# Kernel tuning notes

Measured on AMD Instinct MI355X. Metric: run time of the kernel, lower is better.

Reference implementation:

```python
import jax, jax.numpy as jnp
from jax import lax
import numpy as np

# Module hyperparameters (match init_kwargs)
N = 4            # number of multiplex cells per feature map
NUM_FM = 64      # feature maps in the input
NF = N * NUM_FM  # lateral channel count = 256
H = W = 32       # feature map height/width
D = 2            # lateral neighborhood radius
PRD = 2          # padding repair distance (must equal D for symmetric pad)
KS = 2 * D + 1   # lateral kernel size = 5
IOTA = 0.1       # blend of activation vs lateral support for winner selection
B = 16           # batch size


def minmax_fm(x):
    """Min-max normalize each feature map (over the last two dims) to [0,1].
    Degenerate (constant) maps map to 0."""
    mn = jnp.min(x, axis=(-2, -1), keepdims=True)
    mx = jnp.max(x, axis=(-2, -1), keepdims=True)
    denom = mx - mn
    safe = jnp.where(denom > 0, denom, 1.0)
    return jnp.where(denom > 0, (x - mn) / safe, 0.0)


def _pad(A):
    # pad_activations: zeros of shape (.., PRD+D+H, PRD+D+W), A at [PRD:-PRD]
    # with PRD == D this is symmetric (PRD, D) padding.
    return jnp.pad(A, ((0, 0), (0, 0), (PRD, D), (PRD, D)))


def _conv(x, w):
    # x: (B, Cin, H', W'), w: (Cout, Cin, KS, KS) -> VALID conv (padding=0)
    return lax.conv_general_dilated(x, w, (1, 1), 'VALID',
                                    dimension_numbers=('NCHW', 'OIHW', 'NCHW'))


def setup_inputs() -> dict:
    key = jax.random.key(0)
    k1, k2 = jax.random.split(key)
    A = jax.random.uniform(k1, (B, NUM_FM, H, W), dtype=jnp.float32)
    K = jax.random.normal(k2, (NF, NF, KS, KS), dtype=jnp.float32)  # trained lateral kernel
    S = jnp.ones((NF,), dtype=jnp.float32)                          # scaling param
    return {"A": A, "K": K, "S": S}


def reference(A, K, S):
    batch = A.shape[0]
    # A.repeat(1, n, 1, 1): tile input n times along channels -> (B, NF, H, W)
    A_rep = jnp.tile(A, (1, N, 1, 1))

    # First lateral pass: conv with minmax-normalized K^T, scaled by S, minmaxed.
    L1 = _conv(_pad(A_rep), minmax_fm(jnp.swapaxes(K, 0, 1))) / NUM_FM
    L1 = L1 * S[None, :, None, None]
    L1 = minmax_fm(L1)

    # Winner-take-all multiplex selection (deterministic branch):
    s = jnp.sum((1.0 - IOTA) * A_rep + IOTA * L1, axis=(-2, -1))  # (B, NF)
    s = jnp.swapaxes(s.reshape(batch, N, NUM_FM), 1, 2)            # (B, NUM_FM, N)
    A_max = jnp.argmax(s, axis=-1)                                  # (B, NUM_FM)
    fm_idx = NUM_FM * A_max + jnp.arange(NUM_FM)                    # (B, NUM_FM) channel ids

    # Active-channel mask (complement = inactive_multiplex_idx in the original)
    active = jnp.zeros((batch, NF), dtype=bool)
    active = active.at[jnp.arange(batch)[:, None], fm_idx].set(True)

    # Zero inactive channels of A (tmp_A) and diagonal K[i,i] for inactive i
    # (large_K[b, idx, idx] = 0 is pairwise/diagonal fancy indexing in torch).
    tmp_A = A_rep * active[:, :, None, None].astype(A_rep.dtype)
    eye = jnp.eye(NF, dtype=bool)
    kill = eye[None, :, :] & (~active)[:, :, None]                  # (B, NF, NF)
    large_K = jnp.where(kill[..., None, None], 0.0, K[None])        # (B, NF, NF, KS, KS)

    # Second lateral pass: per-sample conv with per-sample kernel.
    pA = _pad(tmp_A)

    def per_sample(x, Kb):
        w = minmax_fm(jnp.swapaxes(Kb, 0, 1))
        return _conv(x[None], w)[0]

    L2 = jax.vmap(per_sample)(pA, large_K) / NUM_FM                 # (B, NF, H, W)

    # Gather winning channels: filtered_L (B, NUM_FM, H, W)
    return jnp.take_along_axis(L2, fm_idx[:, :, None, None], axis=1)
```

## Files before the change

kernel.cpp:

```cpp
#include <hip/hip_runtime.h>


#define NFM 64
#define NMX 4
#define NFC 256
#define HW 1024
#define KK 25

typedef unsigned short u16;
typedef short short8 __attribute__((ext_vector_type(8)));
typedef float f32x4 __attribute__((ext_vector_type(4)));

__device__ __forceinline__ u16 f2bfbits(float f) {
    unsigned int u = __float_as_uint(f);
    u += 0x7fffu + ((u >> 16) & 1u);
    return (u16)(u >> 16);
}
__device__ __forceinline__ float bf2f(u16 v) {
    return __uint_as_float(((unsigned int)v) << 16);
}

__global__ __launch_bounds__(256) void kprep(const float* __restrict__ K,
                                             float* __restrict__ wsum2) {
    __shared__ __align__(16) float buf[64 * KK];
    int g = blockIdx.x & 63, o0 = (blockIdx.x >> 6) * 64;
    int t = threadIdx.x;
    float wacc[KK];
#pragma unroll
    for (int k = 0; k < KK; ++k) wacc[k] = 0.f;

    for (int n = 0; n < NMX; ++n) {
        int i = n * NFM + g;
        const float4* src = (const float4*)(K + (i * NFC + o0) * KK);
        __syncthreads();
        ((float4*)buf)[t] = src[t];
        if (t < 144) ((float4*)buf)[t + 256] = src[t + 256];
        __syncthreads();
        if (t < 64) {
            float v[KK];
            float mn = 1e30f, mx = -1e30f;
#pragma unroll
            for (int k = 0; k < KK; ++k) {
                v[k] = buf[t * KK + k];
                mn = fminf(mn, v[k]);
                mx = fmaxf(mx, v[k]);
            }
            float d = mx - mn;
            float r = d > 0.f ? 1.f / d : 0.f;
#pragma unroll
            for (int k = 0; k < KK; ++k) wacc[k] += (v[k] - mn) * r;
        }
    }
    __syncthreads();
    if (t < 64) {
#pragma unroll
        for (int k = 0; k < KK; ++k) buf[t * KK + k] = wacc[k];
    }
    __syncthreads();
    for (int idx = t; idx < 1600; idx += 256) {
        int k = idx >> 6, ol = idx & 63;
        wsum2[(g * KK + k) * NFC + o0 + ol] = buf[ol * KK + k];
    }
}

__global__ __launch_bounds__(256) void kpackW(const float* __restrict__ wsum2,
                                              char* __restrict__ Wpk) {
    __shared__ float wlds[64 * 16];
    int dydx = blockIdx.x, ot = blockIdx.y, t = threadIdx.x;
    int o15 = t & 15, gq = t >> 4;
#pragma unroll
    for (int e = 0; e < 4; ++e) {
        int g = e * 16 + gq;
        wlds[g * 16 + o15] = wsum2[(g * KK + dydx) * NFC + ot * 16 + o15];
    }
    __syncthreads();
    int gh = t >> 7, l = t & 63;
    int quad = l >> 4, oo = l & 15;
    short8 hs, ls;
#pragma unroll
    for (int j = 0; j < 8; ++j) {
        float v = wlds[(gh * 32 + quad * 8 + j) * 16 + oo];
        u16 h = f2bfbits(v);
        hs[j] = (short)h;
        ls[j] = (short)f2bfbits(v - bf2f(h));
    }
    char* cb = Wpk + (ot * 50 + dydx * 2 + gh) * 2048 + l * 16;
    *(short8*)cb = hs;
    *(short8*)(cb + 1024) = ls;
}

__global__ __launch_bounds__(512, 2) void kscore(const float* __restrict__ A,
                                                 const char* __restrict__ Wpk,
                                                 float4* __restrict__ part) {
    __shared__ u16 slabh[6 * 36 * 72];
    __shared__ u16 slabl[6 * 36 * 72];
    int t = threadIdx.x;
    int y2 = blockIdx.x, b = blockIdx.y;
    int y0 = y2 * 2;
    int lane = t & 63;
    int wv = __builtin_amdgcn_readfirstlane(t >> 6);
    int n15 = lane & 15, quad = lane >> 4;

    const float* Ab = A + b * NFM * HW;
    for (int ry = 0; ry < 6; ++ry) {
        int gy = y0 - 2 + ry;
        bool rowok = (gy >= 0) && (gy < 32);
        for (int c = 0; c < 5; ++c) {
            int id2 = c * 512 + t;
            if (id2 < 2304) {
                int g = (id2 * 3641) >> 17;
                int xi = id2 - g * 36;
                float v = 0.f;
                if (rowok && xi >= 2 && xi < 34)
                    v = Ab[g * HW + gy * 32 + xi - 2];
                u16 h = f2bfbits(v);
                u16 l = f2bfbits(v - bf2f(h));
                int idx = (ry * 36 + xi) * 72 + g;
                slabh[idx] = h;
                slabl[idx] = l;
            }
        }
    }
    __syncthreads();

    f32x4 acc[2][4];
#pragma unroll
    for (int m = 0; m < 2; ++m)
#pragma unroll
        for (int p = 0; p < 4; ++p)
#pragma unroll
            for (int r = 0; r < 4; ++r) acc[m][p][r] = 0.f;

    const char* wbase0 = Wpk + (wv * 2) * 50 * 2048 + lane * 16;
    const char* wbase1 = wbase0 + 50 * 2048;
    short8 cah0 = *(const short8*)(wbase0);
    short8 cal0 = *(const short8*)(wbase0 + 1024);
    short8 cah1 = *(const short8*)(wbase1);
    short8 cal1 = *(const short8*)(wbase1 + 1024);

    for (int ks = 0; ks < 50; ++ks) {
        int ksn = ks < 49 ? ks + 1 : 49;
        const char* nb0 = wbase0 + (ksn << 11);
        const char* nb1 = wbase1 + (ksn << 11);
        short8 nah0 = *(const short8*)nb0;
        short8 nal0 = *(const short8*)(nb0 + 1024);
        short8 nah1 = *(const short8*)nb1;
        short8 nal1 = *(const short8*)(nb1 + 1024);

        int dydx = ks >> 1;
        int gh = (ks & 1) * 32;
        int dy = dydx / 5, dx = dydx - dy * 5;
        short8 bh[4], bl[4];
#pragma unroll
        for (int p = 0; p < 4; ++p) {
            int r = p >> 1, nt = p & 1;
            int addr = ((r + dy) * 36 + nt * 16 + n15 + dx) * 72 + gh + quad * 8;
            bh[p] = *(const short8*)(slabh + addr);
            bl[p] = *(const short8*)(slabl + addr);
        }
#pragma unroll
        for (int p = 0; p < 4; ++p) {
            acc[0][p] = __builtin_amdgcn_mfma_f32_16x16x32_bf16(cah0, bh[p], acc[0][p], 0, 0, 0);
            acc[0][p] = __builtin_amdgcn_mfma_f32_16x16x32_bf16(cah0, bl[p], acc[0][p], 0, 0, 0);
            acc[0][p] = __builtin_amdgcn_mfma_f32_16x16x32_bf16(cal0, bh[p], acc[0][p], 0, 0, 0);
            acc[1][p] = __builtin_amdgcn_mfma_f32_16x16x32_bf16(cah1, bh[p], acc[1][p], 0, 0, 0);
            acc[1][p] = __builtin_amdgcn_mfma_f32_16x16x32_bf16(cah1, bl[p], acc[1][p], 0, 0, 0);
            acc[1][p] = __builtin_amdgcn_mfma_f32_16x16x32_bf16(cal1, bh[p], acc[1][p], 0, 0, 0);
        }
        cah0 = nah0; cal0 = nal0; cah1 = nah1; cal1 = nal1;
    }

#pragma unroll
    for (int m = 0; m < 2; ++m) {
#pragma unroll
        for (int reg = 0; reg < 4; ++reg) {
            float v0 = acc[m][0][reg], v1 = acc[m][1][reg];
            float v2 = acc[m][2][reg], v3 = acc[m][3][reg];
            float mn = fminf(fminf(v0, v1), fminf(v2, v3));
            float mx = fmaxf(fmaxf(v0, v1), fmaxf(v2, v3));
            float sm = (v0 + v1) + (v2 + v3);
#pragma unroll
            for (int msk = 1; msk <= 8; msk <<= 1) {
                mn = fminf(mn, __shfl_xor(mn, msk, 64));
                mx = fmaxf(mx, __shfl_xor(mx, msk, 64));
                sm += __shfl_xor(sm, msk, 64);
            }
            if (n15 == 0) {
                int o = (wv * 2 + m) * 16 + quad * 4 + reg;
                part[(b * NFC + o) * 16 + y2] = make_float4(mn, mx, sm, 0.f);
            }
        }
    }
}

__global__ __launch_bounds__(256) void kpackO(const float* __restrict__ K,
                                              const float4* __restrict__ part,
                                              const float* __restrict__ S,
                                              char* __restrict__ Wob) {
    __shared__ float scl[NFC];
    __shared__ int igL[NFM];
    __shared__ __align__(16) char cbuf[25 * 2048];
    int ft = blockIdx.x, b = blockIdx.y;
    int t = threadIdx.x;
    {
        const float4* pp = part + (b * NFC + t) * 16;
        float mn = 1e30f, mx = -1e30f, sm = 0.f;
#pragma unroll
        for (int r = 0; r < 16; ++r) {
            float4 p = pp[r];
            mn = fminf(mn, p.x);
            mx = fmaxf(mx, p.y);
            sm += p.z;
        }
        float s = S[t] * (1.f / 64.f);
        float mnv = (s >= 0.f ? mn : mx) * s;
        float mxv = (s >= 0.f ? mx : mn) * s;
        float smv = sm * s;
        float d = mxv - mnv;
        scl[t] = d > 0.f ? (smv - 1024.f * mnv) / d : 0.f;
    }
    __syncthreads();
    if (t < NFM) {
        float best = scl[t];
        int bi = 0;
#pragma unroll
        for (int n = 1; n < NMX; ++n) {
            float v = scl[n * NFM + t];
            if (v > best) { best = v; bi = n; }
        }
        igL[t] = bi * NFM + t;
    }
    __syncthreads();

    int g32 = t & 31, fh = t >> 5;
    int quad = g32 >> 3, j = g32 & 7;
    char* wdst = Wob + b * 409600 + ft * 102400;

    for (int half = 0; half < 2; ++half) {
        int i = igL[half * 32 + g32];
#pragma unroll
        for (int e = 0; e < 2; ++e) {
            int f15 = fh * 2 + e;
            int o = igL[ft * 16 + f15];
            const float* src = K + (i * NFC + o) * KK;
            float v[KK];
            float mn = 1e30f, mx = -1e30f;
#pragma unroll
            for (int k = 0; k < KK; ++k) {
                v[k] = src[k];
                mn = fminf(mn, v[k]);
                mx = fmaxf(mx, v[k]);
            }
            float d = mx - mn;
            float r = d > 0.f ? 1.f / d : 0.f;
            char* base = cbuf + (quad * 16 + f15) * 16 + j * 2;
#pragma unroll
            for (int k = 0; k < KK; ++k) {
                float nv = (v[k] - mn) * r;
                u16 h = f2bfbits(nv);
                u16 l = f2bfbits(nv - bf2f(h));
                *(u16*)(base + k * 2048) = h;
                *(u16*)(base + k * 2048 + 1024) = l;
            }
        }
        __syncthreads();
        for (int idx = t; idx < 3200; idx += 256) {
            int ch = idx >> 7, w = idx & 127;
            *(float4*)(wdst + (ch * 2 + half) * 2048 + w * 16) =
                *(const float4*)(cbuf + ch * 2048 + w * 16);
        }
        __syncthreads();
    }
}

__global__ __launch_bounds__(256, 4) void kout(const float* __restrict__ A,
                                               const char* __restrict__ Wob,
                                               float* __restrict__ out) {
    __shared__ u16 slabh[6 * 20 * 72];
    __shared__ u16 slabl[6 * 20 * 72];
    int t = threadIdx.x;
    int xh = blockIdx.x, yb2 = blockIdx.y, b = blockIdx.z;
    int y0 = yb2 * 2, x0 = xh * 16;
    int lane = t & 63;
    int wv = __builtin_amdgcn_readfirstlane(t >> 6);
    int n15 = lane & 15, quad = lane >> 4;

    const float* Ab = A + b * NFM * HW;
    for (int ry = 0; ry < 6; ++ry) {
        int gy = y0 - 2 + ry;
        bool rowok = (gy >= 0) && (gy < 32);
        for (int c = 0; c < 5; ++c) {
            int id2 = c * 256 + t;
            int g = (id2 * 6554) >> 17;
            int xi = id2 - g * 20;
            int x = x0 + xi - 2;
            float v = 0.f;
            if (rowok && x >= 0 && x < 32)
                v = Ab[g * HW + gy * 32 + x];
            u16 h = f2bfbits(v);
            u16 l = f2bfbits(v - bf2f(h));
            int idx = (ry * 20 + xi) * 72 + g;
            slabh[idx] = h;
            slabl[idx] = l;
        }
    }
    __syncthreads();

    f32x4 acc[2];
#pragma unroll
    for (int r = 0; r < 2; ++r)
#pragma unroll
        for (int jr = 0; jr < 4; ++jr) acc[r][jr] = 0.f;

    const char* wbase = Wob + b * 409600 + (wv * 50) * 2048 + lane * 16;
    short8 cah = *(const short8*)(wbase);
    short8 cal = *(const short8*)(wbase + 1024);

    for (int ks = 0; ks < 50; ++ks) {
        int ksn = ks < 49 ? ks + 1 : 49;
        const char* nb = wbase + (ksn << 11);
        short8 nah = *(const short8*)nb;
        short8 nal = *(const short8*)(nb + 1024);

        int dydx = ks >> 1;
        int gh = (ks & 1) * 32;
        int dy = dydx / 5, dx = dydx - dy * 5;
#pragma unroll
        for (int r = 0; r < 2; ++r) {
            int addr = ((r + dy) * 20 + n15 + dx) * 72 + gh + quad * 8;
            short8 bh = *(const short8*)(slabh + addr);
            short8 bl = *(const short8*)(slabl + addr);
            acc[r] = __builtin_amdgcn_mfma_f32_16x16x32_bf16(cah, bh, acc[r], 0, 0, 0);
            acc[r] = __builtin_amdgcn_mfma_f32_16x16x32_bf16(cah, bl, acc[r], 0, 0, 0);
            acc[r] = __builtin_amdgcn_mfma_f32_16x16x32_bf16(cal, bh, acc[r], 0, 0, 0);
        }
        cah = nah;
        cal = nal;
    }

#pragma unroll
    for (int r = 0; r < 2; ++r)
#pragma unroll
        for (int reg = 0; reg < 4; ++reg) {
            int f = wv * 16 + quad * 4 + reg;
            out[(b * NFM + f) * HW + (y0 + r) * 32 + x0 + n15] = acc[r][reg] * (1.f / 64.f);
        }
}

extern "C" void kernel_launch(void* const* d_in, const int* in_sizes, int n_in,
                              void* d_out, int out_size, void* d_ws, size_t ws_size,
                              hipStream_t stream) {
    const float* A = (const float*)d_in[0];
    const float* K = (const float*)d_in[1];
    const float* S = (const float*)d_in[2];
    float* out = (float*)d_out;

    char* ws = (char*)d_ws;
    char*   Wob   = ws;
    char*   Wpk   = ws;
    float*  wsum2 = (float*)(ws + 1638400);
    float4* part  = (float4*)(ws + 6553600);

    kprep<<<dim3(256), dim3(256), 0, stream>>>(K, wsum2);
    kpackW<<<dim3(25, 16), dim3(256), 0, stream>>>(wsum2, Wpk);
    kscore<<<dim3(16, 16), dim3(512), 0, stream>>>(A, Wpk, part);
    kpackO<<<dim3(4, 16), dim3(256), 0, stream>>>(K, part, S, Wob);
    kout<<<dim3(2, 16, 16), dim3(256), 0, stream>>>(A, Wob, out);
}
```

Before: 150.0 us.

## Split kscore output rows across twice as many waves with LDS reduction

Doubles kscore block size to 1024 threads (16 waves), with each wave computing one output row instead of two. This halves per-wave MFMA work and accumulator registers, and the per-row min/max/sum partials are combined through a shared-memory reduction. It also adds a periodic block barrier every eight k-steps, apparently to keep waves in step on shared weight loads. The change trades more waves per block and extra synchronization for better latency hiding, while weight fragments are now loaded redundantly by two waves.

```diff
diff --git a/kernel.cpp b/kernel.cpp
--- a/kernel.cpp
+++ b/kernel.cpp
@@ -89,24 +89,27 @@
     *(short8*)(cb + 1024) = ls;
 }
 
-__global__ __launch_bounds__(512, 2) void kscore(const float* __restrict__ A,
-                                                 const char* __restrict__ Wpk,
-                                                 float4* __restrict__ part) {
+__global__ __launch_bounds__(1024, 4) void kscore(const float* __restrict__ A,
+                                                  const char* __restrict__ Wpk,
+                                                  float4* __restrict__ part) {
     __shared__ u16 slabh[6 * 36 * 72];
     __shared__ u16 slabl[6 * 36 * 72];
+    __shared__ float4 red[2][NFC];
     int t = threadIdx.x;
     int y2 = blockIdx.x, b = blockIdx.y;
     int y0 = y2 * 2;
     int lane = t & 63;
     int wv = __builtin_amdgcn_readfirstlane(t >> 6);
     int n15 = lane & 15, quad = lane >> 4;
+    int mt = wv & 7;
+    int rh = wv >> 3;
 
     const float* Ab = A + b * NFM * HW;
     for (int ry = 0; ry < 6; ++ry) {
         int gy = y0 - 2 + ry;
         bool rowok = (gy >= 0) && (gy < 32);
-        for (int c = 0; c < 5; ++c) {
-            int id2 = c * 512 + t;
+        for (int c = 0; c < 3; ++c) {
+            int id2 = c * 1024 + t;
             if (id2 < 2304) {
                 int g = (id2 * 3641) >> 17;
                 int xi = id2 - g * 36;
@@ -123,15 +126,15 @@
     }
     __syncthreads();
 
-    f32x4 acc[2][4];
+    f32x4 acc[2][2];
 #pragma unroll
     for (int m = 0; m < 2; ++m)
 #pragma unroll
-        for (int p = 0; p < 4; ++p)
-#pragma unroll
-            for (int r = 0; r < 4; ++r) acc[m][p][r] = 0.f;
-
-    const char* wbase0 = Wpk + (wv * 2) * 50 * 2048 + lane * 16;
+        for (int pl = 0; pl < 2; ++pl)
+#pragma unroll
+            for (int r = 0; r < 4; ++r) acc[m][pl][r] = 0.f;
+
+    const char* wbase0 = Wpk + (mt * 2) * 50 * 2048 + lane * 16;
     const char* wbase1 = wbase0 + 50 * 2048;
     short8 cah0 = *(const short8*)(wbase0);
     short8 cal0 = *(const short8*)(wbase0 + 1024);
@@ -150,24 +153,24 @@
         int dydx = ks >> 1;
         int gh = (ks & 1) * 32;
         int dy = dydx / 5, dx = dydx - dy * 5;
-        short8 bh[4], bl[4];
-#pragma unroll
-        for (int p = 0; p < 4; ++p) {
-            int r = p >> 1, nt = p & 1;
-            int addr = ((r + dy) * 36 + nt * 16 + n15 + dx) * 72 + gh + quad * 8;
-            bh[p] = *(const short8*)(slabh + addr);
-            bl[p] = *(const short8*)(slabl + addr);
-        }
-#pragma unroll
-        for (int p = 0; p < 4; ++p) {
-            acc[0][p] = __builtin_amdgcn_mfma_f32_16x16x32_bf16(cah0, bh[p], acc[0][p], 0, 0, 0);
-            acc[0][p] = __builtin_amdgcn_mfma_f32_16x16x32_bf16(cah0, bl[p], acc[0][p], 0, 0, 0);
-            acc[0][p] = __builtin_amdgcn_mfma_f32_16x16x32_bf16(cal0, bh[p], acc[0][p], 0, 0, 0);
-            acc[1][p] = __builtin_amdgcn_mfma_f32_16x16x32_bf16(cah1, bh[p], acc[1][p], 0, 0, 0);
-            acc[1][p] = __builtin_amdgcn_mfma_f32_16x16x32_bf16(cah1, bl[p], acc[1][p], 0, 0, 0);
-            acc[1][p] = __builtin_amdgcn_mfma_f32_16x16x32_bf16(cal1, bh[p], acc[1][p], 0, 0, 0);
+        short8 bh[2], bl[2];
+#pragma unroll
+        for (int pl = 0; pl < 2; ++pl) {
+            int addr = ((rh + dy) * 36 + pl * 16 + n15 + dx) * 72 + gh + quad * 8;
+            bh[pl] = *(const short8*)(slabh + addr);
+            bl[pl] = *(const short8*)(slabl + addr);
+        }
+#pragma unroll
+        for (int pl = 0; pl < 2; ++pl) {
+            acc[0][pl] = __builtin_amdgcn_mfma_f32_16x16x32_bf16(cah0, bh[pl], acc[0][pl], 0, 0, 0);
+            acc[0][pl] = __builtin_amdgcn_mfma_f32_16x16x32_bf16(cah0, bl[pl], acc[0][pl], 0, 0, 0);
+            acc[0][pl] = __builtin_amdgcn_mfma_f32_16x16x32_bf16(cal0, bh[pl], acc[0][pl], 0, 0, 0);
+            acc[1][pl] = __builtin_amdgcn_mfma_f32_16x16x32_bf16(cah1, bh[pl], acc[1][pl], 0, 0, 0);
+            acc[1][pl] = __builtin_amdgcn_mfma_f32_16x16x32_bf16(cah1, bl[pl], acc[1][pl], 0, 0, 0);
+            acc[1][pl] = __builtin_amdgcn_mfma_f32_16x16x32_bf16(cal1, bh[pl], acc[1][pl], 0, 0, 0);
         }
         cah0 = nah0; cal0 = nal0; cah1 = nah1; cal1 = nal1;
+        if ((ks & 7) == 7) __syncthreads();
     }
 
 #pragma unroll
@@ -175,10 +178,9 @@
 #pragma unroll
         for (int reg = 0; reg < 4; ++reg) {
             float v0 = acc[m][0][reg], v1 = acc[m][1][reg];
-            float v2 = acc[m][2][reg], v3 = acc[m][3][reg];
-            float mn = fminf(fminf(v0, v1), fminf(v2, v3));
-            float mx = fmaxf(fmaxf(v0, v1), fmaxf(v2, v3));
-            float sm = (v0 + v1) + (v2 + v3);
+            float mn = fminf(v0, v1);
+            float mx = fmaxf(v0, v1);
+            float sm = v0 + v1;
 #pragma unroll
             for (int msk = 1; msk <= 8; msk <<= 1) {
                 mn = fminf(mn, __shfl_xor(mn, msk, 64));
@@ -186,10 +188,16 @@
                 sm += __shfl_xor(sm, msk, 64);
             }
             if (n15 == 0) {
-                int o = (wv * 2 + m) * 16 + quad * 4 + reg;
-                part[(b * NFC + o) * 16 + y2] = make_float4(mn, mx, sm, 0.f);
-            }
-        }
+                int o = (mt * 2 + m) * 16 + quad * 4 + reg;
+                red[rh][o] = make_float4(mn, mx, sm, 0.f);
+            }
+        }
+    }
+    __syncthreads();
+    if (t < NFC) {
+        float4 r0 = red[0][t], r1 = red[1][t];
+        part[(b * NFC + t) * 16 + y2] =
+            make_float4(fminf(r0.x, r1.x), fmaxf(r0.y, r1.y), r0.z + r1.z, 0.f);
     }
 }
 
@@ -363,7 +371,7 @@
 
     kprep<<<dim3(256), dim3(256), 0, stream>>>(K, wsum2);
     kpackW<<<dim3(25, 16), dim3(256), 0, stream>>>(wsum2, Wpk);
-    kscore<<<dim3(16, 16), dim3(512), 0, stream>>>(A, Wpk, part);
+    kscore<<<dim3(16, 16), dim3(1024), 0, stream>>>(A, Wpk, part);
     kpackO<<<dim3(4, 16), dim3(256), 0, stream>>>(K, part, S, Wob);
     kout<<<dim3(2, 16, 16), dim3(256), 0, stream>>>(A, Wob, out);
 }
```

Measured after the change: 154.6 us. +3.1%, slower.
